# Performance work log

Measured on AMD Instinct MI355X. Metric: run time of the kernel, lower is better.

The kernel has to match this reference:

```python
import jax, jax.numpy as jnp
import numpy as np

WINDOW_LEN = 19  # hardcoded in original module
N_MFCC = 30      # hardcoded in original module


def setup_inputs() -> dict:
    key = jax.random.key(0)
    # [batch, time, n_mfcc]
    x = jax.random.normal(key, (32, 4096, N_MFCC), dtype=jnp.float32)
    return {"x": x}


def reference(x):
    """Overlapping time-window extraction.

    The original performs conv1d(x, eye(W*C) filter, stride=1, SAME) then
    reshapes to [B, T, W, C]. With an identity filter this is exactly:
        out[b, t, w, c] = x_zeropad[b, t + w - W//2, c]
    We implement it as the equivalent (and FLOP-free) strided gather.
    """
    B, T, C = x.shape
    pad = WINDOW_LEN // 2  # SAME padding for odd filter width -> 9 each side
    xp = jnp.pad(x, ((0, 0), (pad, pad), (0, 0)))
    # idx[t, w] = t + w, indexing into padded time axis
    idx = jnp.arange(T)[:, None] + jnp.arange(WINDOW_LEN)[None, :]  # [T, W]
    out = xp[:, idx, :]  # [B, T, W, C]
    return out
```

## Files before the change

### kernel.cpp

```cpp
#include <hip/hip_runtime.h>


typedef float f32x4 __attribute__((ext_vector_type(4)));

constexpr int B   = 32;
constexpr int T   = 4096;
constexpr int C   = 30;
constexpr int PAD = 9;
constexpr int ROW = 570;
constexpr int TC  = T * C;
constexpr int PAIR_F4 = 285;
constexpr unsigned NPAIRS = (unsigned)B * (T / 2);
constexpr unsigned TOTAL4 = NPAIRS * PAIR_F4;

__global__ __launch_bounds__(256)
void OverlapTimeWindowLayer_kernel(const float* __restrict__ x,
                                   f32x4* __restrict__ out) {
    const unsigned v = blockIdx.x * 256u + threadIdx.x;
    const unsigned p = v / PAIR_F4;
    const int u  = (int)(v - p * PAIR_F4);
    const int b  = (int)(p >> 11);
    const int tp = (int)(p & 2047);
    const int base = (2 * tp - PAD) * C;
    const int e0 = 4 * u;
    const float* xb = x + (unsigned)b * TC;

    const int s0 = base + e0     - (e0     >= ROW ? (ROW - C) : 0);
    const int s1 = base + e0 + 2 - (e0 + 2 >= ROW ? (ROW - C) : 0);

    float2 lo = make_float2(0.0f, 0.0f);
    float2 hi = make_float2(0.0f, 0.0f);
    if (s0 >= 0 && s0 < TC) lo = *reinterpret_cast<const float2*>(xb + s0);
    if (s1 >= 0 && s1 < TC) hi = *reinterpret_cast<const float2*>(xb + s1);

    f32x4 val;
    val.x = lo.x; val.y = lo.y; val.z = hi.x; val.w = hi.y;
    out[v] = val;
}

extern "C" void kernel_launch(void* const* d_in, const int* in_sizes, int n_in,
                              void* d_out, int out_size, void* d_ws, size_t ws_size,
                              hipStream_t stream) {
    const float* x = (const float*)d_in[0];
    f32x4* out = (f32x4*)d_out;
    const int block = 256;
    const unsigned grid = TOTAL4 / block;
    OverlapTimeWindowLayer_kernel<<<grid, block, 0, stream>>>(x, out);
}
```

Baseline: 64.63 us.

## Stage input time tiles in LDS and emit windows with nontemporal stores

Each workgroup now covers 128 time steps of one batch. It loads the padded input slab (146 rows of 30 floats) into shared memory once, then builds all the overlapping window outputs from LDS. This replaces the roughly 19x redundant global/L2 reads of the input with LDS reads, and it writes the output with nontemporal stores to avoid polluting the cache. In exchange the grid is much smaller (1024 workgroups), each thread loops over many outputs, and a barrier now sits between the load and store phases.

```diff
diff --git a/kernel.cpp b/kernel.cpp
--- a/kernel.cpp
+++ b/kernel.cpp
@@ -9,33 +9,49 @@
 constexpr int PAD = 9;
 constexpr int ROW = 570;
 constexpr int TC  = T * C;
-constexpr int PAIR_F4 = 285;
-constexpr unsigned NPAIRS = (unsigned)B * (T / 2);
-constexpr unsigned TOTAL4 = NPAIRS * PAIR_F4;
+constexpr int TB  = 128;
+constexpr int SROWS   = TB + 2 * PAD;
+constexpr int SFLOATS = SROWS * C;
+constexpr int S2      = SFLOATS / 2;
+constexpr int OUT_F4  = TB / 2 * 285;
+constexpr unsigned NWG = (unsigned)B * (T / TB);
 
 __global__ __launch_bounds__(256)
 void OverlapTimeWindowLayer_kernel(const float* __restrict__ x,
                                    f32x4* __restrict__ out) {
-    const unsigned v = blockIdx.x * 256u + threadIdx.x;
-    const unsigned p = v / PAIR_F4;
-    const int u  = (int)(v - p * PAIR_F4);
-    const int b  = (int)(p >> 11);
-    const int tp = (int)(p & 2047);
-    const int base = (2 * tp - PAD) * C;
-    const int e0 = 4 * u;
+    __shared__ float lds[SFLOATS];
+
+    const unsigned blk = blockIdx.x;
+    const int b  = (int)(blk >> 5);
+    const int t0 = (int)(blk & 31u) * TB;
     const float* xb = x + (unsigned)b * TC;
+    const int sbase = (t0 - PAD) * C;
 
-    const int s0 = base + e0     - (e0     >= ROW ? (ROW - C) : 0);
-    const int s1 = base + e0 + 2 - (e0 + 2 >= ROW ? (ROW - C) : 0);
+    for (int j = (int)threadIdx.x; j < S2; j += 256) {
+        const int s = sbase + 2 * j;
+        float2 v = make_float2(0.0f, 0.0f);
+        if (s >= 0 && s < TC) v = *reinterpret_cast<const float2*>(xb + s);
+        *reinterpret_cast<float2*>(lds + 2 * j) = v;
+    }
+    __syncthreads();
 
-    float2 lo = make_float2(0.0f, 0.0f);
-    float2 hi = make_float2(0.0f, 0.0f);
-    if (s0 >= 0 && s0 < TC) lo = *reinterpret_cast<const float2*>(xb + s0);
-    if (s1 >= 0 && s1 < TC) hi = *reinterpret_cast<const float2*>(xb + s1);
+    f32x4* outb = out + blk * (unsigned)OUT_F4;
+#pragma unroll 2
+    for (int i = (int)threadIdx.x; i < OUT_F4; i += 256) {
+        const int rp = i / 285;
+        const int u  = i - rp * 285;
+        const int e0 = 4 * u;
+        const int f  = rp * 60 + e0;
+        const int f0 = f     - (e0     >= ROW ? (ROW - C) : 0);
+        const int f1 = f + 2 - (e0 + 2 >= ROW ? (ROW - C) : 0);
 
-    f32x4 val;
-    val.x = lo.x; val.y = lo.y; val.z = hi.x; val.w = hi.y;
-    out[v] = val;
+        const float2 lo = *reinterpret_cast<const float2*>(lds + f0);
+        const float2 hi = *reinterpret_cast<const float2*>(lds + f1);
+
+        f32x4 val;
+        val.x = lo.x; val.y = lo.y; val.z = hi.x; val.w = hi.y;
+        __builtin_nontemporal_store(val, outb + i);
+    }
 }
 
 extern "C" void kernel_launch(void* const* d_in, const int* in_sizes, int n_in,
@@ -43,7 +59,5 @@
                               hipStream_t stream) {
     const float* x = (const float*)d_in[0];
     f32x4* out = (f32x4*)d_out;
-    const int block = 256;
-    const unsigned grid = TOTAL4 / block;
-    OverlapTimeWindowLayer_kernel<<<grid, block, 0, stream>>>(x, out);
+    OverlapTimeWindowLayer_kernel<<<NWG, 256, 0, stream>>>(x, out);
 }
```

Result: no change. 65.60 us (+1.5%).
